# Performance work log

Measured on AMD Instinct MI355X. Metric: run time of the kernel, lower is better.

## Reference

```python
import jax, jax.numpy as jnp
import numpy as np

D_MODEL = 1024
HEADS = 16
D_HEAD = D_MODEL // HEADS
CAUSAL = True


def setup_inputs() -> dict:
    key = jax.random.key(0)
    ks = jax.random.split(key, 11)
    B, L = 4, 2048
    s = 1.0 / np.sqrt(D_MODEL)
    inp = {
        'q': jax.random.normal(ks[0], (B, L, D_MODEL), jnp.float32),
        'k': jax.random.normal(ks[1], (B, L, D_MODEL), jnp.float32),
        'v': jax.random.normal(ks[2], (B, L, D_MODEL), jnp.float32),
        'Wq': jax.random.normal(ks[3], (D_MODEL, D_MODEL), jnp.float32) * s,
        'bq': jnp.zeros((D_MODEL,), jnp.float32),
        'Wk': jax.random.normal(ks[4], (D_MODEL, D_MODEL), jnp.float32) * s,
        'bk': jnp.zeros((D_MODEL,), jnp.float32),
        'Wv': jax.random.normal(ks[5], (D_MODEL, D_MODEL), jnp.float32) * s,
        'bv': jnp.zeros((D_MODEL,), jnp.float32),
        'Wo': jax.random.normal(ks[6], (D_MODEL, D_MODEL), jnp.float32) * s,
        'bo': jnp.zeros((D_MODEL,), jnp.float32),
    }
    return inp


def _split(x):
    B, L, _ = x.shape
    return x.reshape(B, L, HEADS, D_HEAD).transpose(0, 2, 1, 3)  # [B,H,L,Dh]


def reference(q, k, v, Wq, bq, Wk, bk, Wv, bv, Wo, bo):
    qh = _split(q @ Wq + bq)
    kh = _split(k @ Wk + bk)
    vh = _split(v @ Wv + bv)
    scores = jnp.einsum('bhqd,bhkd->bhqk', qh, kh) / jnp.sqrt(jnp.float32(D_HEAD))
    if CAUSAL:
        Lq, Lk = q.shape[1], k.shape[1]
        mask = jnp.triu(jnp.ones((Lq, Lk), bool), k=1)
        scores = jnp.where(mask[None, None], -jnp.inf, scores)
    attn = jax.nn.softmax(scores, axis=-1)
    out = jnp.einsum('bhqk,bhkd->bhqd', attn, vh)
    B, H, L, Dh = out.shape
    out = out.transpose(0, 2, 1, 3).reshape(B, L, H * Dh)
    return out @ Wo + bo
```

## Files before the change

### kernel.cpp

```cpp
#include <hip/hip_runtime.h>

#define DM 1024
#define HEADS 16
#define DH 64
#define BB 4
#define LL 2048
#define MROWS (BB * LL)

typedef __bf16 bf16x8 __attribute__((ext_vector_type(8)));
typedef float f32x4 __attribute__((ext_vector_type(4)));
typedef float f32x16 __attribute__((ext_vector_type(16)));

__device__ __forceinline__ unsigned short f2bf(float f) {
  __bf16 h = (__bf16)f;
  return __builtin_bit_cast(unsigned short, h);
}
__device__ __forceinline__ unsigned int pack2(float a, float b) {
  return (unsigned int)f2bf(a) | ((unsigned int)f2bf(b) << 16);
}

__device__ __forceinline__ void gload16(const unsigned short* g, unsigned short* l) {
  __builtin_amdgcn_global_load_lds(
      (const __attribute__((address_space(1))) unsigned int*)(const void*)g,
      (__attribute__((address_space(3))) unsigned int*)(void*)l, 16, 0, 0);
}

__global__ __launch_bounds__(256) void transpose_w_kernel(
    const float* __restrict__ W0, const float* __restrict__ W1,
    const float* __restrict__ W2, const float* __restrict__ W3,
    unsigned short* __restrict__ T0, unsigned short* __restrict__ T1,
    unsigned short* __restrict__ T2, unsigned short* __restrict__ T3) {
  const float* Wt[4] = {W0, W1, W2, W3};
  unsigned short* Tt[4] = {T0, T1, T2, T3};
  const float* W = Wt[blockIdx.z];
  unsigned short* WT = Tt[blockIdx.z];
  __shared__ float tile[32][33];
  const int tx = threadIdx.x & 31;
  const int ty = threadIdx.x >> 5;
  const int x0 = blockIdx.x * 32;
  const int y0 = blockIdx.y * 32;
#pragma unroll
  for (int i = 0; i < 32; i += 8)
    tile[ty + i][tx] = W[(size_t)(y0 + ty + i) * DM + x0 + tx];
  __syncthreads();
#pragma unroll
  for (int i = 0; i < 32; i += 8)
    WT[(size_t)(x0 + ty + i) * DM + y0 + tx] = f2bf(tile[tx][ty + i]);
}

__global__ __launch_bounds__(256) void cvt_bf16_kernel(
    const float* __restrict__ x, unsigned short* __restrict__ y) {
  const size_t i = ((size_t)blockIdx.x * 256 + threadIdx.x) * 8;
  float4 a = *(const float4*)(x + i);
  float4 b = *(const float4*)(x + i + 4);
  uint4 p = {pack2(a.x, a.y), pack2(a.z, a.w), pack2(b.x, b.y), pack2(b.z, b.w)};
  *(uint4*)(y + i) = p;
}

template <int OUTMODE>
__global__ __launch_bounds__(256) void gemm_bf16_kernel(
    const unsigned short* __restrict__ A, const unsigned short* __restrict__ BT,
    const float* __restrict__ bias, void* __restrict__ Cptr, float scale) {
  constexpr int K = DM, N = DM;
  __shared__ unsigned short As[128 * 32];
  __shared__ unsigned short Bs[128 * 32];
  const int t = threadIdx.x;
  const int lane = t & 63;
  const int w = t >> 6;
  const int wr = w >> 1, wc = w & 1;
  const int fr = lane & 15, kg = lane >> 4;

  const int flat = blockIdx.y * gridDim.x + blockIdx.x;
  const int cpx = (gridDim.x * gridDim.y) >> 3;
  const int swz = (flat & 7) * cpx + (flat >> 3);
  const int m0 = (swz / gridDim.x) * 128;
  const int n0 = (swz % gridDim.x) * 128;

  const int grow = lane >> 2, gcol8 = (lane & 3) * 8;

  f32x4 acc[4][4] = {};

  for (int kt = 0; kt < K / 32; ++kt) {
    const int k0 = kt * 32;
#pragma unroll
    for (int i = 0; i < 2; i++) {
      gload16(A + (size_t)(m0 + i * 64 + w * 16 + grow) * K + k0 + gcol8,
              &As[(i * 256 + w * 64 + lane) * 8]);
      gload16(BT + (size_t)(n0 + i * 64 + w * 16 + grow) * K + k0 + gcol8,
              &Bs[(i * 256 + w * 64 + lane) * 8]);
    }
    __syncthreads();

    bf16x8 af[4], bfr[4];
#pragma unroll
    for (int i = 0; i < 4; i++)
      af[i] = *(const bf16x8*)&As[(wr * 64 + i * 16 + fr) * 32 + kg * 8];
#pragma unroll
    for (int i = 0; i < 4; i++)
      bfr[i] = *(const bf16x8*)&Bs[(wc * 64 + i * 16 + fr) * 32 + kg * 8];
#pragma unroll
    for (int i = 0; i < 4; i++)
#pragma unroll
      for (int j = 0; j < 4; j++)
        acc[i][j] = __builtin_amdgcn_mfma_f32_16x16x32_bf16(af[i], bfr[j], acc[i][j], 0, 0, 0);
    __syncthreads();
  }

#pragma unroll
  for (int j = 0; j < 4; j++) {
    const int gcol = n0 + wc * 64 + j * 16 + fr;
    const float bv = bias[gcol];
    const int h = gcol >> 6, dh = gcol & 63;
#pragma unroll
    for (int i = 0; i < 4; i++) {
      const int grow0 = m0 + wr * 64 + i * 16 + kg * 4;
      if (OUTMODE == 2) {
        const int b = grow0 >> 11, l = grow0 & 2047;
        uint2 pk;
        pk.x = pack2(acc[i][j][0] + bv, acc[i][j][1] + bv);
        pk.y = pack2(acc[i][j][2] + bv, acc[i][j][3] + bv);
        *(uint2*)((unsigned short*)Cptr +
                  ((size_t)((b * HEADS + h) * DH + dh)) * LL + l) = pk;
      } else {
#pragma unroll
        for (int r = 0; r < 4; r++) {
          const int grow2 = grow0 + r;
          if (OUTMODE == 0) {
            const float val = (acc[i][j][r] + bv) * scale;
            const int b = grow2 >> 11, l = grow2 & 2047;
            ((unsigned short*)Cptr)[(((size_t)(b * HEADS + h) * LL + l) << 6) + dh] = f2bf(val);
          } else {
            ((float*)Cptr)[(size_t)grow2 * N + gcol] = acc[i][j][r] + bv;
          }
        }
      }
    }
  }
}

#define QSCALE 0.18033688011112042f

#define PAD 78
__global__ __launch_bounds__(256, 4) void attn_kernel(
    const unsigned short* __restrict__ Qh, const unsigned short* __restrict__ Kh,
    const unsigned short* __restrict__ VhT, unsigned short* __restrict__ O) {
  __shared__ unsigned short Ks[2][64][PAD];
  __shared__ unsigned short VTs[2][64][PAD];
  const int t = threadIdx.x, lane = t & 63, w = t >> 6;
  const int lo5 = lane & 31, hi = lane >> 5;

  const int f = (int)(blockIdx.y * gridDim.x + blockIdx.x);
  const int l = f >> 8;
  const int c = f & 255;
  const int xcd = c & 7, j = c >> 3;
  const int bh = xcd * 8 + (j & 7);
  const int sub = j >> 3;
  const int qi = (l == 0) ? sub : (l == 1) ? 7 - sub : (l == 2) ? 8 + sub : 15 - sub;

  const size_t base = (size_t)bh * LL * DH;
  const unsigned short* Kb = Kh + base;
  const unsigned short* Vb = VhT + base;

  const int rA = t >> 3, kA = (t & 7) * 8;
  const int rB = rA + 32;

  const int b = bh >> 4, h = bh & 15;

  const int q0 = qi * 128;
  const int qrow = q0 + w * 32 + lo5;

  bf16x8 qf[4];
  {
    const unsigned short* Qb = Qh + base + (size_t)qrow * DH + hi * 8;
#pragma unroll
    for (int kc = 0; kc < 4; kc++) qf[kc] = *(const bf16x8*)(Qb + kc * 16);
  }

  float m_run = -INFINITY, l_run = 0.f;
  f32x16 oacc[2] = {};

  const int ntiles = 2 * (qi + 1);
  const int my_last = (q0 + w * 32 + 31) >> 6;

  uint4 kr0 = *(const uint4*)(Kb + (size_t)rA * DH + kA);
  uint4 kr1 = *(const uint4*)(Kb + (size_t)rB * DH + kA);
  uint4 vr0 = *(const uint4*)(Vb + (size_t)rA * LL + kA);
  uint4 vr1 = *(const uint4*)(Vb + (size_t)rB * LL + kA);
  *(uint4*)&Ks[0][rA][kA] = kr0;
  *(uint4*)&Ks[0][rB][kA] = kr1;
  *(uint4*)&VTs[0][rA][kA] = vr0;
  *(uint4*)&VTs[0][rB][kA] = vr1;

  for (int jt = 0; jt < ntiles; ++jt) {
    const int cur = jt & 1;
    if (jt + 1 < ntiles) {
      const int kv1 = (jt + 1) * 64;
      kr0 = *(const uint4*)(Kb + (size_t)(kv1 + rA) * DH + kA);
      kr1 = *(const uint4*)(Kb + (size_t)(kv1 + rB) * DH + kA);
      vr0 = *(const uint4*)(Vb + (size_t)rA * LL + kv1 + kA);
      vr1 = *(const uint4*)(Vb + (size_t)rB * LL + kv1 + kA);
    }
    __syncthreads();

    if (jt <= my_last) {
      f32x16 s2[2] = {};
      __builtin_amdgcn_s_setprio(1);
#pragma unroll
      for (int tt = 0; tt < 2; tt++)
#pragma unroll
        for (int kc = 0; kc < 4; kc++) {
          bf16x8 kf = *(const bf16x8*)&Ks[cur][tt * 32 + lo5][kc * 16 + hi * 8];
          s2[tt] = __builtin_amdgcn_mfma_f32_32x32x16_bf16(kf, qf[kc], s2[tt], 0, 0, 0);
        }
      __builtin_amdgcn_s_setprio(0);

      const int kv0 = jt * 64;
      if (kv0 + 63 > q0 + w * 32) {
        const int thr = qrow - kv0 - 4 * hi;
#pragma unroll
        for (int tt = 0; tt < 2; tt++)
#pragma unroll
          for (int i = 0; i < 16; i++) {
            const int kvoff = tt * 32 + (i & 3) + 8 * (i >> 2);
            s2[tt][i] = (kvoff > thr) ? -1e30f : s2[tt][i];
          }
      }

      float mx;
      {
        float m8[8];
#pragma unroll
        for (int i = 0; i < 8; i++)
          m8[i] = fmaxf(fmaxf(s2[0][i], s2[0][i + 8]), fmaxf(s2[1][i], s2[1][i + 8]));
#pragma unroll
        for (int st = 4; st > 0; st >>= 1)
#pragma unroll
          for (int i = 0; i < st; i++) m8[i] = fmaxf(m8[i], m8[i + st]);
        mx = m8[0];
      }
      mx = fmaxf(mx, __shfl_xor(mx, 32));

      if (__any(mx > m_run + 8.0f)) {
        const float mnew = fmaxf(m_run, mx);
        const float corr = __builtin_amdgcn_exp2f(m_run - mnew);
        m_run = mnew;
        l_run *= corr;
#pragma unroll
        for (int od = 0; od < 2; od++)
#pragma unroll
          for (int i = 0; i < 16; i++) oacc[od][i] *= corr;
      }

#pragma unroll
      for (int tt = 0; tt < 2; tt++)
#pragma unroll
        for (int i = 0; i < 16; i++)
          s2[tt][i] = __builtin_amdgcn_exp2f(s2[tt][i] - m_run);

      float rs;
      {
        float a8[8];
#pragma unroll
        for (int i = 0; i < 8; i++)
          a8[i] = (s2[0][i] + s2[0][i + 8]) + (s2[1][i] + s2[1][i + 8]);
#pragma unroll
        for (int st = 4; st > 0; st >>= 1)
#pragma unroll
          for (int i = 0; i < st; i++) a8[i] += a8[i + st];
        rs = a8[0];
      }
      rs += __shfl_xor(rs, 32);
      l_run += rs;

      union U8 { uint4 u; bf16x8 v; } pa[4];
#pragma unroll
      for (int ks = 0; ks < 4; ks++) {
        const int tt = ks >> 1, b0 = (ks & 1) * 8;
        const unsigned int w0 = pack2(s2[tt][b0 + 0], s2[tt][b0 + 1]);
        const unsigned int w1 = pack2(s2[tt][b0 + 2], s2[tt][b0 + 3]);
        const unsigned int w2 = pack2(s2[tt][b0 + 4], s2[tt][b0 + 5]);
        const unsigned int w3 = pack2(s2[tt][b0 + 6], s2[tt][b0 + 7]);
        const unsigned int p0 = (unsigned int)__shfl_xor((int)w0, 32);
        const unsigned int p1 = (unsigned int)__shfl_xor((int)w1, 32);
        const unsigned int p2 = (unsigned int)__shfl_xor((int)w2, 32);
        const unsigned int p3 = (unsigned int)__shfl_xor((int)w3, 32);
        pa[ks].u = hi ? make_uint4(p2, p3, w2, w3) : make_uint4(w0, w1, p0, p1);
      }

      __builtin_amdgcn_s_setprio(1);
#pragma unroll
      for (int od = 0; od < 2; od++)
#pragma unroll
        for (int ks = 0; ks < 4; ks++) {
          bf16x8 vf = *(const bf16x8*)&VTs[cur][od * 32 + lo5][ks * 16 + hi * 8];
          oacc[od] = __builtin_amdgcn_mfma_f32_32x32x16_bf16(vf, pa[ks].v, oacc[od], 0, 0, 0);
        }
      __builtin_amdgcn_s_setprio(0);
    }

    if (jt + 1 < ntiles) {
      *(uint4*)&Ks[cur ^ 1][rA][kA] = kr0;
      *(uint4*)&Ks[cur ^ 1][rB][kA] = kr1;
      *(uint4*)&VTs[cur ^ 1][rA][kA] = vr0;
      *(uint4*)&VTs[cur ^ 1][rB][kA] = vr1;
    }
  }

  const float linv = 1.f / l_run;
  unsigned short* Ob = O + ((size_t)(b * LL + qrow) * DM) + h * DH;
#pragma unroll
  for (int od = 0; od < 2; od++)
#pragma unroll
    for (int m = 0; m < 8; m++) {
      const int dh0 = od * 32 + ((2 * m) & 3) + 8 * ((2 * m) >> 2) + 4 * hi;
      const unsigned int pk =
          pack2(oacc[od][2 * m] * linv, oacc[od][2 * m + 1] * linv);
      *(unsigned int*)(Ob + dh0) = pk;
    }
}

extern "C" void kernel_launch(void* const* d_in, const int* in_sizes, int n_in,
                              void* d_out, int out_size, void* d_ws, size_t ws_size,
                              hipStream_t stream) {
  (void)in_sizes; (void)n_in; (void)out_size; (void)ws_size;
  const float* q  = (const float*)d_in[0];
  const float* k  = (const float*)d_in[1];
  const float* v  = (const float*)d_in[2];
  const float* Wq = (const float*)d_in[3];
  const float* bq = (const float*)d_in[4];
  const float* Wk = (const float*)d_in[5];
  const float* bk = (const float*)d_in[6];
  const float* Wv = (const float*)d_in[7];
  const float* bv = (const float*)d_in[8];
  const float* Wo = (const float*)d_in[9];
  const float* bo = (const float*)d_in[10];

  char* ws = (char*)d_ws;
  const size_t WSZ = (size_t)DM * DM * 2;
  const size_t HSZ = (size_t)MROWS * DM * 2;
  unsigned short* WqT = (unsigned short*)(ws);
  unsigned short* WkT = (unsigned short*)(ws + WSZ);
  unsigned short* WvT = (unsigned short*)(ws + 2 * WSZ);
  unsigned short* WoT = (unsigned short*)(ws + 3 * WSZ);
  unsigned short* Qh  = (unsigned short*)(ws + 4 * WSZ);
  unsigned short* Kh  = (unsigned short*)(ws + 4 * WSZ + HSZ);
  unsigned short* VhT = (unsigned short*)(ws + 4 * WSZ + 2 * HSZ);
  unsigned short* X   = (unsigned short*)(ws + 4 * WSZ + 3 * HSZ);
  unsigned short* Oc  = X;

  transpose_w_kernel<<<dim3(32, 32, 4), 256, 0, stream>>>(
      Wq, Wk, Wv, Wo, WqT, WkT, WvT, WoT);

  const dim3 cgrid(MROWS * DM / (256 * 8));
  const dim3 ggrid(DM / 128, MROWS / 128);

  cvt_bf16_kernel<<<cgrid, 256, 0, stream>>>(q, X);
  gemm_bf16_kernel<0><<<ggrid, 256, 0, stream>>>(X, WqT, bq, Qh, QSCALE);
  cvt_bf16_kernel<<<cgrid, 256, 0, stream>>>(k, X);
  gemm_bf16_kernel<0><<<ggrid, 256, 0, stream>>>(X, WkT, bk, Kh, 1.0f);
  cvt_bf16_kernel<<<cgrid, 256, 0, stream>>>(v, X);
  gemm_bf16_kernel<2><<<ggrid, 256, 0, stream>>>(X, WvT, bv, VhT, 1.0f);

  attn_kernel<<<dim3(16, BB * HEADS), 256, 0, stream>>>(Qh, Kh, VhT, Oc);

  gemm_bf16_kernel<1><<<ggrid, 256, 0, stream>>>(Oc, WoT, bo, (float*)d_out, 1.0f);
}
```

Before: 218.9 us.

## Batch QKV conversion and projections into single launches, deepen GEMM K-tile

Merges the three fp32-to-bf16 conversions and the three Q/K/V projection GEMMs into one batched launch each, using a z grid dimension, when the workspace is large enough. The GEMM K tile grows from 32 to 64, which halves the number of barriers per output tile but doubles LDS use per block. The attention kernel's LDS padding changes from 78 to 76 and its row-max reduction is rewritten as a flatter tree. Batching the launches gives the GPU more concurrent blocks and removes serialization between the projections, at the cost of extra workspace for separate bf16 copies of q, k and v.

```diff
diff --git a/kernel.cpp b/kernel.cpp
--- a/kernel.cpp
+++ b/kernel.cpp
@@ -57,13 +57,27 @@
   *(uint4*)(y + i) = p;
 }
 
+__global__ __launch_bounds__(256) void cvt3_bf16_kernel(
+    const float* __restrict__ q, const float* __restrict__ k,
+    const float* __restrict__ v, unsigned short* __restrict__ Xq,
+    unsigned short* __restrict__ Xk, unsigned short* __restrict__ Xv) {
+  const int z = blockIdx.y;
+  const float* x = (z == 0) ? q : (z == 1) ? k : v;
+  unsigned short* y = (z == 0) ? Xq : (z == 1) ? Xk : Xv;
+  const size_t i = ((size_t)blockIdx.x * 256 + threadIdx.x) * 8;
+  float4 a = *(const float4*)(x + i);
+  float4 b = *(const float4*)(x + i + 4);
+  uint4 p = {pack2(a.x, a.y), pack2(a.z, a.w), pack2(b.x, b.y), pack2(b.z, b.w)};
+  *(uint4*)(y + i) = p;
+}
+
 template <int OUTMODE>
-__global__ __launch_bounds__(256) void gemm_bf16_kernel(
+__device__ __forceinline__ void gemm_body64(
     const unsigned short* __restrict__ A, const unsigned short* __restrict__ BT,
     const float* __restrict__ bias, void* __restrict__ Cptr, float scale) {
   constexpr int K = DM, N = DM;
-  __shared__ unsigned short As[128 * 32];
-  __shared__ unsigned short Bs[128 * 32];
+  __shared__ unsigned short As[128 * 64];
+  __shared__ unsigned short Bs[128 * 64];
   const int t = threadIdx.x;
   const int lane = t & 63;
   const int w = t >> 6;
@@ -76,33 +90,36 @@
   const int m0 = (swz / gridDim.x) * 128;
   const int n0 = (swz % gridDim.x) * 128;
 
-  const int grow = lane >> 2, gcol8 = (lane & 3) * 8;
+  const int srow = t >> 3, scol = (t & 7) * 8;
 
   f32x4 acc[4][4] = {};
 
-  for (int kt = 0; kt < K / 32; ++kt) {
-    const int k0 = kt * 32;
-#pragma unroll
-    for (int i = 0; i < 2; i++) {
-      gload16(A + (size_t)(m0 + i * 64 + w * 16 + grow) * K + k0 + gcol8,
-              &As[(i * 256 + w * 64 + lane) * 8]);
-      gload16(BT + (size_t)(n0 + i * 64 + w * 16 + grow) * K + k0 + gcol8,
-              &Bs[(i * 256 + w * 64 + lane) * 8]);
+  for (int kt = 0; kt < K / 64; ++kt) {
+    const int k0 = kt * 64;
+#pragma unroll
+    for (int i = 0; i < 4; i++) {
+      gload16(A + (size_t)(m0 + i * 32 + srow) * K + k0 + scol,
+              &As[(i * 256 + t) * 8]);
+      gload16(BT + (size_t)(n0 + i * 32 + srow) * K + k0 + scol,
+              &Bs[(i * 256 + t) * 8]);
     }
     __syncthreads();
 
-    bf16x8 af[4], bfr[4];
-#pragma unroll
-    for (int i = 0; i < 4; i++)
-      af[i] = *(const bf16x8*)&As[(wr * 64 + i * 16 + fr) * 32 + kg * 8];
-#pragma unroll
-    for (int i = 0; i < 4; i++)
-      bfr[i] = *(const bf16x8*)&Bs[(wc * 64 + i * 16 + fr) * 32 + kg * 8];
-#pragma unroll
-    for (int i = 0; i < 4; i++)
-#pragma unroll
-      for (int j = 0; j < 4; j++)
-        acc[i][j] = __builtin_amdgcn_mfma_f32_16x16x32_bf16(af[i], bfr[j], acc[i][j], 0, 0, 0);
+#pragma unroll
+    for (int ks = 0; ks < 2; ks++) {
+      bf16x8 af[4], bfr[4];
+#pragma unroll
+      for (int i = 0; i < 4; i++)
+        af[i] = *(const bf16x8*)&As[(wr * 64 + i * 16 + fr) * 64 + ks * 32 + kg * 8];
+#pragma unroll
+      for (int i = 0; i < 4; i++)
+        bfr[i] = *(const bf16x8*)&Bs[(wc * 64 + i * 16 + fr) * 64 + ks * 32 + kg * 8];
+#pragma unroll
+      for (int i = 0; i < 4; i++)
+#pragma unroll
+        for (int j = 0; j < 4; j++)
+          acc[i][j] = __builtin_amdgcn_mfma_f32_16x16x32_bf16(af[i], bfr[j], acc[i][j], 0, 0, 0);
+    }
     __syncthreads();
   }
 
@@ -140,7 +157,29 @@
 
 #define QSCALE 0.18033688011112042f
 
-#define PAD 78
+__global__ __launch_bounds__(256) void qkv_gemm_kernel(
+    const unsigned short* __restrict__ A0, size_t strideA,
+    const unsigned short* __restrict__ WT0,
+    const float* __restrict__ bq, const float* __restrict__ bk,
+    const float* __restrict__ bv, unsigned short* __restrict__ O0, int zoff) {
+  const int z = (int)blockIdx.z + zoff;
+  const unsigned short* A = A0 + (size_t)z * strideA;
+  const unsigned short* BT = WT0 + (size_t)z * DM * DM;
+  const float* bias = (z == 0) ? bq : (z == 1) ? bk : bv;
+  unsigned short* C = O0 + (size_t)z * MROWS * DM;
+  if (z == 2)
+    gemm_body64<2>(A, BT, bias, C, 1.0f);
+  else
+    gemm_body64<0>(A, BT, bias, C, (z == 0) ? QSCALE : 1.0f);
+}
+
+__global__ __launch_bounds__(256) void oproj_gemm_kernel(
+    const unsigned short* __restrict__ Oc, const unsigned short* __restrict__ WoT,
+    const float* __restrict__ bo, float* __restrict__ out) {
+  gemm_body64<1>(Oc, WoT, bo, out, 1.0f);
+}
+
+#define PAD 76
 __global__ __launch_bounds__(256, 4) void attn_kernel(
     const unsigned short* __restrict__ Qh, const unsigned short* __restrict__ Kh,
     const unsigned short* __restrict__ VhT, unsigned short* __restrict__ O) {
@@ -232,11 +271,10 @@
 #pragma unroll
         for (int i = 0; i < 8; i++)
           m8[i] = fmaxf(fmaxf(s2[0][i], s2[0][i + 8]), fmaxf(s2[1][i], s2[1][i + 8]));
-#pragma unroll
-        for (int st = 4; st > 0; st >>= 1)
-#pragma unroll
-          for (int i = 0; i < st; i++) m8[i] = fmaxf(m8[i], m8[i + st]);
-        mx = m8[0];
+        const float a3 = fmaxf(fmaxf(m8[0], m8[1]), m8[2]);
+        const float b3 = fmaxf(fmaxf(m8[3], m8[4]), m8[5]);
+        const float c3 = fmaxf(m8[6], m8[7]);
+        mx = fmaxf(fmaxf(a3, b3), c3);
       }
       mx = fmaxf(mx, __shfl_xor(mx, 32));
 
@@ -322,7 +360,7 @@
 extern "C" void kernel_launch(void* const* d_in, const int* in_sizes, int n_in,
                               void* d_out, int out_size, void* d_ws, size_t ws_size,
                               hipStream_t stream) {
-  (void)in_sizes; (void)n_in; (void)out_size; (void)ws_size;
+  (void)in_sizes; (void)n_in; (void)out_size;
   const float* q  = (const float*)d_in[0];
   const float* k  = (const float*)d_in[1];
   const float* v  = (const float*)d_in[2];
@@ -338,9 +376,7 @@
   char* ws = (char*)d_ws;
   const size_t WSZ = (size_t)DM * DM * 2;
   const size_t HSZ = (size_t)MROWS * DM * 2;
-  unsigned short* WqT = (unsigned short*)(ws);
-  unsigned short* WkT = (unsigned short*)(ws + WSZ);
-  unsigned short* WvT = (unsigned short*)(ws + 2 * WSZ);
+  unsigned short* WT0 = (unsigned short*)(ws);
   unsigned short* WoT = (unsigned short*)(ws + 3 * WSZ);
   unsigned short* Qh  = (unsigned short*)(ws + 4 * WSZ);
   unsigned short* Kh  = (unsigned short*)(ws + 4 * WSZ + HSZ);
@@ -349,19 +385,31 @@
   unsigned short* Oc  = X;
 
   transpose_w_kernel<<<dim3(32, 32, 4), 256, 0, stream>>>(
-      Wq, Wk, Wv, Wo, WqT, WkT, WvT, WoT);
+      Wq, Wk, Wv, Wo,
+      WT0, WT0 + DM * DM, WT0 + 2 * (size_t)DM * DM, WoT);
 
   const dim3 cgrid(MROWS * DM / (256 * 8));
   const dim3 ggrid(DM / 128, MROWS / 128);
-
-  cvt_bf16_kernel<<<cgrid, 256, 0, stream>>>(q, X);
-  gemm_bf16_kernel<0><<<ggrid, 256, 0, stream>>>(X, WqT, bq, Qh, QSCALE);
-  cvt_bf16_kernel<<<cgrid, 256, 0, stream>>>(k, X);
-  gemm_bf16_kernel<0><<<ggrid, 256, 0, stream>>>(X, WkT, bk, Kh, 1.0f);
-  cvt_bf16_kernel<<<cgrid, 256, 0, stream>>>(v, X);
-  gemm_bf16_kernel<2><<<ggrid, 256, 0, stream>>>(X, WvT, bv, VhT, 1.0f);
+  const size_t NEED = 4 * WSZ + 6 * HSZ;
+
+  if (ws_size >= NEED) {
+    unsigned short* Xq = X;
+    unsigned short* Xk = X + (size_t)MROWS * DM;
+    unsigned short* Xv = X + 2 * (size_t)MROWS * DM;
+    cvt3_bf16_kernel<<<dim3(MROWS * DM / (256 * 8), 3), 256, 0, stream>>>(
+        q, k, v, Xq, Xk, Xv);
+    qkv_gemm_kernel<<<dim3(DM / 128, MROWS / 128, 3), 256, 0, stream>>>(
+        Xq, (size_t)MROWS * DM, WT0, bq, bk, bv, Qh, 0);
+  } else {
+    cvt_bf16_kernel<<<cgrid, 256, 0, stream>>>(q, X);
+    qkv_gemm_kernel<<<ggrid, 256, 0, stream>>>(X, 0, WT0, bq, bk, bv, Qh, 0);
+    cvt_bf16_kernel<<<cgrid, 256, 0, stream>>>(k, X);
+    qkv_gemm_kernel<<<ggrid, 256, 0, stream>>>(X, 0, WT0, bq, bk, bv, Qh, 1);
+    cvt_bf16_kernel<<<cgrid, 256, 0, stream>>>(v, X);
+    qkv_gemm_kernel<<<ggrid, 256, 0, stream>>>(X, 0, WT0, bq, bk, bv, Qh, 2);
+  }
 
   attn_kernel<<<dim3(16, BB * HEADS), 256, 0, stream>>>(Qh, Kh, VhT, Oc);
 
-  gemm_bf16_kernel<1><<<ggrid, 256, 0, stream>>>(Oc, WoT, bo, (float*)d_out, 1.0f);
-}
+  oproj_gemm_kernel<<<ggrid, 256, 0, stream>>>(Oc, WoT, bo, (float*)d_out);
+}
```

After: 213.9 us. -2.3%, faster.
